# Kernel optimization log

Measured on AMD Instinct MI355X. Metric: run time of the kernel, lower is better.

## Reference

```python
import jax, jax.numpy as jnp
import numpy as np

N_HEAD = 32
HEAD_DIM = 32  # must equal N_HEAD due to the module's einsum index reuse
N_EMBD = N_HEAD * HEAD_DIM
VOCAB = 32000
B, T = 2, 64
TEMP_MIN = 0.1


def setup_inputs() -> dict:
    key = jax.random.key(0)
    ks = jax.random.split(key, 8)
    inv = 1.0 / np.sqrt(HEAD_DIM)
    return {
        "x": jax.random.normal(ks[0], (B, T, N_EMBD), dtype=jnp.float32),
        "vocab_emb": jax.random.normal(ks[1], (VOCAB, N_EMBD), dtype=jnp.float32) * 0.02,
        "W_ffn": jax.random.normal(ks[2], (HEAD_DIM, HEAD_DIM), dtype=jnp.float32) * inv,
        "b_ffn": jnp.zeros((HEAD_DIM,), dtype=jnp.float32),
        "temps": jnp.ones((N_HEAD,), dtype=jnp.float32),
        "W_ref": jax.random.normal(ks[3], (HEAD_DIM, HEAD_DIM), dtype=jnp.float32) * inv,
        "b_ref": jnp.zeros((HEAD_DIM,), dtype=jnp.float32),
        "W_gate": jax.random.normal(ks[4], (HEAD_DIM, HEAD_DIM), dtype=jnp.float32) * inv,
        "b_gate": jnp.zeros((HEAD_DIM,), dtype=jnp.float32),
    }


def reference(x, vocab_emb, W_ffn, b_ffn, temps, W_ref, b_ref, W_gate, b_gate):
    Bs, Ts, C = x.shape
    # per-head channel decomposition: (B*T, n_head, head_dim)
    xc = x.reshape(Bs * Ts, N_HEAD, HEAD_DIM)
    # channel_ffns: shared Linear over the head_dim axis (torch Linear: x @ W.T + b)
    ffn = jnp.einsum('bnh,dh->bnd', xc, W_ffn) + b_ffn
    # vocab channels: (n_head, vocab, head_dim)
    vc = vocab_emb.reshape(VOCAB, N_HEAD, HEAD_DIM).transpose(1, 0, 2)
    temps_c = jnp.clip(temps, TEMP_MIN, None)[None, :, None]

    def vocab_project(q):
        # faithful to torch: einsum('bnh,hvd->bnv') contracts q's head_dim
        # against vc's HEAD axis and sums over d as well (requires head_dim == n_head)
        logits = jnp.einsum('bnh,hvd->bnv', q, vc)
        w = jax.nn.softmax(logits / temps_c, axis=-1)  # (B*T, n_head, vocab)
        return jnp.einsum('bnv,hvd->bnh', w, vc)

    vocab_out = vocab_project(ffn)  # (B*T, n_head, head_dim)

    # refinement stage (use_vocab_refinement=True)
    refinement = jnp.tanh(jnp.einsum('bnh,dh->bnd', xc, W_ref) + b_ref)
    gate = jax.nn.sigmoid(jnp.einsum('bnh,dh->bnd', xc, W_gate) + b_gate)
    refined = vocab_out * (1.0 - gate) + refinement * gate
    vocab_out = vocab_project(refined)

    # dropout p=0 (eval) -> identity
    return vocab_out.reshape(Bs, Ts, C)
```

## Files before the change

### kernel.cpp

```cpp
#include <hip/hip_runtime.h>
#include <hip/hip_bf16.h>
#include <cstdint>

typedef unsigned int uint;
typedef unsigned short ushort_t;

typedef __attribute__((ext_vector_type(8))) short short8;
typedef __attribute__((ext_vector_type(4))) short short4_t;
typedef __attribute__((ext_vector_type(4))) float float4_t;

#define NEMBD 1024
#define VOCAB 32000
#define LOG2E 1.4426950408889634f

__device__ __forceinline__ ushort_t f2bf_rne(float f) {
    uint u = __float_as_uint(f);
    u += 0x7fffu + ((u >> 16) & 1u);
    return (ushort_t)(u >> 16);
}

__global__ void k_build_st(const float* __restrict__ ve, ushort_t* __restrict__ ST) {
    int v = blockIdx.x;
    int t = threadIdx.x;
    const float4* row = (const float4*)(ve + (size_t)v * NEMBD);
    float4 f = row[t];
    float s = f.x + f.y + f.z + f.w;
    s += __shfl_down(s, 4, 8);
    s += __shfl_down(s, 2, 8);
    s += __shfl_down(s, 1, 8);
    if ((t & 7) == 0) ST[v * 32 + (t >> 3)] = f2bf_rne(s);
}

__global__ void k_pack(const ushort_t* __restrict__ ST, ushort_t* __restrict__ SA,
                       ushort_t* __restrict__ S2) {
    int c = blockIdx.x;
    int t = threadIdx.x;
    if (t < 128) {
        int tile = t >> 6, lane = t & 63;
        int quad = lane >> 4, lo = lane & 15;
        uint4 d = *(const uint4*)(ST + ((size_t)(c * 32 + tile * 16 + lo)) * 32 + quad * 8);
        ((uint4*)SA)[c * 128 + t] = d;
    } else {
        int tt = t - 128;
        int f = tt >> 6, l = tt & 63;
        int quad = l >> 4, lo = l & 15;
        uint w[4];
        #pragma unroll
        for (int t2 = 0; t2 < 2; t2++) {
            #pragma unroll
            for (int jj = 0; jj < 2; jj++) {
                ushort_t v0 = ST[(c * 32 + t2 * 16 + quad * 4 + jj * 2 + 0) * 32 + f * 16 + lo];
                ushort_t v1 = ST[(c * 32 + t2 * 16 + quad * 4 + jj * 2 + 1) * 32 + f * 16 + lo];
                w[t2 * 2 + jj] = (uint)v0 | ((uint)v1 << 16);
            }
        }
        ((uint4*)S2)[c * 128 + tt] = make_uint4(w[0], w[1], w[2], w[3]);
    }
}

__global__ void k_q1(const float* __restrict__ x, const float* __restrict__ W,
                     const float* __restrict__ b, const float* __restrict__ temps,
                     ushort_t* __restrict__ q1) {
    int tid = blockIdx.x * 256 + threadIdx.x;
    int i = tid >> 5, d = tid & 31, n = i & 31;
    const float* xr = x + i * 32;
    float s = b[d];
    #pragma unroll
    for (int h = 0; h < 32; h++) s += xr[h] * W[d * 32 + h];
    q1[tid] = f2bf_rne(s * (LOG2E / fmaxf(temps[n], 0.1f)));
}

__launch_bounds__(256, 8)
__global__ void k_proj(const ushort_t* __restrict__ SA, const ushort_t* __restrict__ S2,
                       const ushort_t* __restrict__ q, float* __restrict__ pN,
                       float* __restrict__ pD) {
    __shared__ ushort_t buf[2][2][2048];
    int g = blockIdx.x >> 5, p = blockIdx.x & 31;
    int w = threadIdx.x >> 6, lane = threadIdx.x & 63;
    int quad = lane >> 4, lo = lane & 15;

    short8 qf = *(const short8*)(q + ((g * 64 + w * 16 + lo) * 32 + quad * 8));

    float4_t pv0 = (float4_t){0.f, 0.f, 0.f, 0.f};
    float4_t pv1 = (float4_t){0.f, 0.f, 0.f, 0.f};
    float dsum = 0.f;
    const float4_t zero4 = (float4_t){0.f, 0.f, 0.f, 0.f};

    int start = (p * 125) >> 2, end = ((p + 1) * 125) >> 2;

    {
        int c = start + (w >> 1);
        if (c < end) {
            const ushort_t* src = ((w & 1) ? S2 : SA) + (size_t)c * 1024;
            uint4 d0 = *(const uint4*)(src + lane * 8);
            uint4 d1 = *(const uint4*)(src + 512 + lane * 8);
            uint4* dst = (uint4*)(&buf[0][w >> 1][(w & 1) * 1024]);
            dst[lane] = d0;
            dst[64 + lane] = d1;
        }
    }
    __syncthreads();

    int ngrp = (end - start + 1) >> 1;
    for (int grp = 0; grp < ngrp; grp++) {
        int cur = grp & 1;
        int cn = start + (grp + 1) * 2 + (w >> 1);
        if (cn < end) {
            const ushort_t* src = ((w & 1) ? S2 : SA) + (size_t)cn * 1024;
            uint4 d0 = *(const uint4*)(src + lane * 8);
            uint4 d1 = *(const uint4*)(src + 512 + lane * 8);
            uint4* dst = (uint4*)(&buf[cur ^ 1][w >> 1][(w & 1) * 1024]);
            dst[lane] = d0;
            dst[64 + lane] = d1;
        }
        int c0 = start + grp * 2;
        int jend = (end - c0 < 2) ? (end - c0) : 2;
        for (int j = 0; j < jend; j++) {
            const ushort_t* sa = &buf[cur][j][0];
            const ushort_t* s2 = &buf[cur][j][1024];
            short8 a0 = *(const short8*)(sa + lane * 8);
            short8 a1 = *(const short8*)(sa + 512 + lane * 8);
            short8 sb0 = *(const short8*)(s2 + lane * 8);
            short8 sb1 = *(const short8*)(s2 + 512 + lane * 8);
            short4_t b00 = {sb0[0], sb0[1], sb0[2], sb0[3]};
            short4_t b01 = {sb0[4], sb0[5], sb0[6], sb0[7]};
            short4_t b10 = {sb1[0], sb1[1], sb1[2], sb1[3]};
            short4_t b11 = {sb1[4], sb1[5], sb1[6], sb1[7]};

            float4_t l0 = __builtin_amdgcn_mfma_f32_16x16x32_bf16(a0, qf, zero4, 0, 0, 0);
            float4_t l1 = __builtin_amdgcn_mfma_f32_16x16x32_bf16(a1, qf, zero4, 0, 0, 0);
            float e0 = __builtin_amdgcn_exp2f(l0[0]);
            float e1 = __builtin_amdgcn_exp2f(l0[1]);
            float e2 = __builtin_amdgcn_exp2f(l0[2]);
            float e3 = __builtin_amdgcn_exp2f(l0[3]);
            float f0 = __builtin_amdgcn_exp2f(l1[0]);
            float f1 = __builtin_amdgcn_exp2f(l1[1]);
            float f2 = __builtin_amdgcn_exp2f(l1[2]);
            float f3 = __builtin_amdgcn_exp2f(l1[3]);
            uint u0 = __builtin_amdgcn_perm(__float_as_uint(e1), __float_as_uint(e0), 0x07060302u);
            uint u1 = __builtin_amdgcn_perm(__float_as_uint(e3), __float_as_uint(e2), 0x07060302u);
            uint u2 = __builtin_amdgcn_perm(__float_as_uint(f1), __float_as_uint(f0), 0x07060302u);
            uint u3 = __builtin_amdgcn_perm(__float_as_uint(f3), __float_as_uint(f2), 0x07060302u);
            dsum += __uint_as_float(u0 << 16) + __uint_as_float(u0 & 0xffff0000u)
                  + __uint_as_float(u1 << 16) + __uint_as_float(u1 & 0xffff0000u)
                  + __uint_as_float(u2 << 16) + __uint_as_float(u2 & 0xffff0000u)
                  + __uint_as_float(u3 << 16) + __uint_as_float(u3 & 0xffff0000u);
            union { uint u[2]; short4_t s4; } c0u, c1u;
            c0u.u[0] = u0; c0u.u[1] = u1;
            c1u.u[0] = u2; c1u.u[1] = u3;
            short4_t P0 = c0u.s4, P1 = c1u.s4;
            pv0 = __builtin_amdgcn_mfma_f32_16x16x16bf16_1k(P0, b00, pv0, 0, 0, 0);
            pv0 = __builtin_amdgcn_mfma_f32_16x16x16bf16_1k(P1, b01, pv0, 0, 0, 0);
            pv1 = __builtin_amdgcn_mfma_f32_16x16x16bf16_1k(P0, b10, pv1, 0, 0, 0);
            pv1 = __builtin_amdgcn_mfma_f32_16x16x16bf16_1k(P1, b11, pv1, 0, 0, 0);
        }
        __syncthreads();
    }

    dsum += __shfl_xor(dsum, 16, 64);
    dsum += __shfl_xor(dsum, 32, 64);

    int gp = blockIdx.x;
    #pragma unroll
    for (int r = 0; r < 4; r++) {
        int ql = w * 16 + quad * 4 + r;
        pN[((size_t)gp * 64 + ql) * 32 + lo]      = pv0[r];
        pN[((size_t)gp * 64 + ql) * 32 + 16 + lo] = pv1[r];
    }
    if (quad == 0) pD[gp * 64 + w * 16 + lo] = dsum;
}

__global__ void k_refine(const float* __restrict__ pN, const float* __restrict__ pD,
                         const float* __restrict__ x,
                         const float* __restrict__ Wr, const float* __restrict__ br,
                         const float* __restrict__ Wg, const float* __restrict__ bg,
                         const float* __restrict__ temps, ushort_t* __restrict__ q2) {
    int tid = blockIdx.x * 256 + threadIdx.x;
    int i = tid >> 5, h = tid & 31, n = i & 31;
    int g = i >> 6, ql = i & 63;
    float N = 0.f, D = 0.f;
    #pragma unroll
    for (int p = 0; p < 32; p++) {
        N += pN[((size_t)(g * 32 + p) * 64 + ql) * 32 + h];
        D += pD[(g * 32 + p) * 64 + ql];
    }
    float vo = N / D;
    const float* xr = x + i * 32;
    float sr = br[h], sg = bg[h];
    #pragma unroll
    for (int h2 = 0; h2 < 32; h2++) {
        sr += xr[h2] * Wr[h * 32 + h2];
        sg += xr[h2] * Wg[h * 32 + h2];
    }
    float ref  = tanhf(sr);
    float gate = 1.f / (1.f + __expf(-sg));
    float refined = vo * (1.f - gate) + ref * gate;
    q2[tid] = f2bf_rne(refined * (LOG2E / fmaxf(temps[n], 0.1f)));
}

__global__ void k_final(const float* __restrict__ pN, const float* __restrict__ pD,
                        float* __restrict__ out) {
    int tid = blockIdx.x * 256 + threadIdx.x;
    int i = tid >> 5, h = tid & 31;
    int g = i >> 6, ql = i & 63;
    float N = 0.f, D = 0.f;
    #pragma unroll
    for (int p = 0; p < 32; p++) {
        N += pN[((size_t)(g * 32 + p) * 64 + ql) * 32 + h];
        D += pD[(g * 32 + p) * 64 + ql];
    }
    out[tid] = N / D;
}

extern "C" void kernel_launch(void* const* d_in, const int* in_sizes, int n_in,
                              void* d_out, int out_size, void* d_ws, size_t ws_size,
                              hipStream_t stream) {
    const float* x     = (const float*)d_in[0];
    const float* ve    = (const float*)d_in[1];
    const float* Wf    = (const float*)d_in[2];
    const float* bfn   = (const float*)d_in[3];
    const float* temps = (const float*)d_in[4];
    const float* Wr    = (const float*)d_in[5];
    const float* br    = (const float*)d_in[6];
    const float* Wg    = (const float*)d_in[7];
    const float* bg    = (const float*)d_in[8];
    float* out = (float*)d_out;

    char* ws = (char*)d_ws;
    ushort_t* ST = (ushort_t*)ws;
    ushort_t* SA = (ushort_t*)(ws + 2048000);
    ushort_t* S2 = (ushort_t*)(ws + 4096000);
    ushort_t* q1 = (ushort_t*)(ws + 6144000);
    ushort_t* q2 = (ushort_t*)(ws + 6144000 + 262144);
    char* base = ws + 6144000 + 2 * 262144;
    float* pNa = (float*)base;
    float* pDa = (float*)(base + 16777216);
    float* pNb = (float*)(base + 16777216 + 524288);
    float* pDb = (float*)(base + 2 * 16777216 + 524288);

    k_build_st<<<dim3(VOCAB), dim3(256), 0, stream>>>(ve, ST);
    k_pack<<<dim3(1000), dim3(256), 0, stream>>>(ST, SA, S2);
    k_q1<<<dim3(512), dim3(256), 0, stream>>>(x, Wf, bfn, temps, q1);
    k_proj<<<dim3(2048), dim3(256), 0, stream>>>(SA, S2, q1, pNa, pDa);
    k_refine<<<dim3(512), dim3(256), 0, stream>>>(pNa, pDa, x, Wr, br, Wg, bg, temps, q2);
    k_proj<<<dim3(2048), dim3(256), 0, stream>>>(SA, S2, q2, pNb, pDb);
    k_final<<<dim3(512), dim3(256), 0, stream>>>(pNb, pDb, out);
}
```

Baseline: 276.4 us.

## Drop LDS staging in k_proj, read vocab tiles directly, reorder block mapping

Removes the double-buffered shared-memory staging and per-group barriers in the projection kernel. Each wave now loads its vocab tile fragments straight from global memory with an unrolled loop. The block index mapping is swapped so that the 64 query groups sharing a vocab partition run as neighbouring blocks, which should improve L2 reuse of the vocab slice. The reduction kernels are updated to the new partial-result layout. The risk is that every wave now issues redundant global loads and loses latency hiding, since the barriers previously kept the waves in step.

New measurement: 286.7 us. +3.7%, slower.

```diff
diff --git a/kernel.cpp b/kernel.cpp
--- a/kernel.cpp
+++ b/kernel.cpp
@@ -74,8 +74,7 @@
 __global__ void k_proj(const ushort_t* __restrict__ SA, const ushort_t* __restrict__ S2,
                        const ushort_t* __restrict__ q, float* __restrict__ pN,
                        float* __restrict__ pD) {
-    __shared__ ushort_t buf[2][2][2048];
-    int g = blockIdx.x >> 5, p = blockIdx.x & 31;
+    int p = blockIdx.x >> 6, g = blockIdx.x & 63;
     int w = threadIdx.x >> 6, lane = threadIdx.x & 63;
     int quad = lane >> 4, lo = lane & 15;
 
@@ -87,74 +86,47 @@
     const float4_t zero4 = (float4_t){0.f, 0.f, 0.f, 0.f};
 
     int start = (p * 125) >> 2, end = ((p + 1) * 125) >> 2;
-
-    {
-        int c = start + (w >> 1);
-        if (c < end) {
-            const ushort_t* src = ((w & 1) ? S2 : SA) + (size_t)c * 1024;
-            uint4 d0 = *(const uint4*)(src + lane * 8);
-            uint4 d1 = *(const uint4*)(src + 512 + lane * 8);
-            uint4* dst = (uint4*)(&buf[0][w >> 1][(w & 1) * 1024]);
-            dst[lane] = d0;
-            dst[64 + lane] = d1;
-        }
-    }
-    __syncthreads();
-
-    int ngrp = (end - start + 1) >> 1;
-    for (int grp = 0; grp < ngrp; grp++) {
-        int cur = grp & 1;
-        int cn = start + (grp + 1) * 2 + (w >> 1);
-        if (cn < end) {
-            const ushort_t* src = ((w & 1) ? S2 : SA) + (size_t)cn * 1024;
-            uint4 d0 = *(const uint4*)(src + lane * 8);
-            uint4 d1 = *(const uint4*)(src + 512 + lane * 8);
-            uint4* dst = (uint4*)(&buf[cur ^ 1][w >> 1][(w & 1) * 1024]);
-            dst[lane] = d0;
-            dst[64 + lane] = d1;
-        }
-        int c0 = start + grp * 2;
-        int jend = (end - c0 < 2) ? (end - c0) : 2;
-        for (int j = 0; j < jend; j++) {
-            const ushort_t* sa = &buf[cur][j][0];
-            const ushort_t* s2 = &buf[cur][j][1024];
-            short8 a0 = *(const short8*)(sa + lane * 8);
-            short8 a1 = *(const short8*)(sa + 512 + lane * 8);
-            short8 sb0 = *(const short8*)(s2 + lane * 8);
-            short8 sb1 = *(const short8*)(s2 + 512 + lane * 8);
-            short4_t b00 = {sb0[0], sb0[1], sb0[2], sb0[3]};
-            short4_t b01 = {sb0[4], sb0[5], sb0[6], sb0[7]};
-            short4_t b10 = {sb1[0], sb1[1], sb1[2], sb1[3]};
-            short4_t b11 = {sb1[4], sb1[5], sb1[6], sb1[7]};
-
-            float4_t l0 = __builtin_amdgcn_mfma_f32_16x16x32_bf16(a0, qf, zero4, 0, 0, 0);
-            float4_t l1 = __builtin_amdgcn_mfma_f32_16x16x32_bf16(a1, qf, zero4, 0, 0, 0);
-            float e0 = __builtin_amdgcn_exp2f(l0[0]);
-            float e1 = __builtin_amdgcn_exp2f(l0[1]);
-            float e2 = __builtin_amdgcn_exp2f(l0[2]);
-            float e3 = __builtin_amdgcn_exp2f(l0[3]);
-            float f0 = __builtin_amdgcn_exp2f(l1[0]);
-            float f1 = __builtin_amdgcn_exp2f(l1[1]);
-            float f2 = __builtin_amdgcn_exp2f(l1[2]);
-            float f3 = __builtin_amdgcn_exp2f(l1[3]);
-            uint u0 = __builtin_amdgcn_perm(__float_as_uint(e1), __float_as_uint(e0), 0x07060302u);
-            uint u1 = __builtin_amdgcn_perm(__float_as_uint(e3), __float_as_uint(e2), 0x07060302u);
-            uint u2 = __builtin_amdgcn_perm(__float_as_uint(f1), __float_as_uint(f0), 0x07060302u);
-            uint u3 = __builtin_amdgcn_perm(__float_as_uint(f3), __float_as_uint(f2), 0x07060302u);
-            dsum += __uint_as_float(u0 << 16) + __uint_as_float(u0 & 0xffff0000u)
-                  + __uint_as_float(u1 << 16) + __uint_as_float(u1 & 0xffff0000u)
-                  + __uint_as_float(u2 << 16) + __uint_as_float(u2 & 0xffff0000u)
-                  + __uint_as_float(u3 << 16) + __uint_as_float(u3 & 0xffff0000u);
-            union { uint u[2]; short4_t s4; } c0u, c1u;
-            c0u.u[0] = u0; c0u.u[1] = u1;
-            c1u.u[0] = u2; c1u.u[1] = u3;
-            short4_t P0 = c0u.s4, P1 = c1u.s4;
-            pv0 = __builtin_amdgcn_mfma_f32_16x16x16bf16_1k(P0, b00, pv0, 0, 0, 0);
-            pv0 = __builtin_amdgcn_mfma_f32_16x16x16bf16_1k(P1, b01, pv0, 0, 0, 0);
-            pv1 = __builtin_amdgcn_mfma_f32_16x16x16bf16_1k(P0, b10, pv1, 0, 0, 0);
-            pv1 = __builtin_amdgcn_mfma_f32_16x16x16bf16_1k(P1, b11, pv1, 0, 0, 0);
-        }
-        __syncthreads();
+    const ushort_t* pa = SA + (size_t)start * 1024 + lane * 8;
+    const ushort_t* pb = S2 + (size_t)start * 1024 + lane * 8;
+
+    #pragma unroll 2
+    for (int c = start; c < end; c++) {
+        short8 a0  = *(const short8*)pa;
+        short8 a1  = *(const short8*)(pa + 512);
+        short8 sb0 = *(const short8*)pb;
+        short8 sb1 = *(const short8*)(pb + 512);
+        pa += 1024; pb += 1024;
+        short4_t b00 = {sb0[0], sb0[1], sb0[2], sb0[3]};
+        short4_t b01 = {sb0[4], sb0[5], sb0[6], sb0[7]};
+        short4_t b10 = {sb1[0], sb1[1], sb1[2], sb1[3]};
+        short4_t b11 = {sb1[4], sb1[5], sb1[6], sb1[7]};
+
+        float4_t l0 = __builtin_amdgcn_mfma_f32_16x16x32_bf16(a0, qf, zero4, 0, 0, 0);
+        float4_t l1 = __builtin_amdgcn_mfma_f32_16x16x32_bf16(a1, qf, zero4, 0, 0, 0);
+        float e0 = __builtin_amdgcn_exp2f(l0[0]);
+        float e1 = __builtin_amdgcn_exp2f(l0[1]);
+        float e2 = __builtin_amdgcn_exp2f(l0[2]);
+        float e3 = __builtin_amdgcn_exp2f(l0[3]);
+        float f0 = __builtin_amdgcn_exp2f(l1[0]);
+        float f1 = __builtin_amdgcn_exp2f(l1[1]);
+        float f2 = __builtin_amdgcn_exp2f(l1[2]);
+        float f3 = __builtin_amdgcn_exp2f(l1[3]);
+        uint u0 = __builtin_amdgcn_perm(__float_as_uint(e1), __float_as_uint(e0), 0x07060302u);
+        uint u1 = __builtin_amdgcn_perm(__float_as_uint(e3), __float_as_uint(e2), 0x07060302u);
+        uint u2 = __builtin_amdgcn_perm(__float_as_uint(f1), __float_as_uint(f0), 0x07060302u);
+        uint u3 = __builtin_amdgcn_perm(__float_as_uint(f3), __float_as_uint(f2), 0x07060302u);
+        dsum += __uint_as_float(u0 << 16) + __uint_as_float(u0 & 0xffff0000u)
+              + __uint_as_float(u1 << 16) + __uint_as_float(u1 & 0xffff0000u)
+              + __uint_as_float(u2 << 16) + __uint_as_float(u2 & 0xffff0000u)
+              + __uint_as_float(u3 << 16) + __uint_as_float(u3 & 0xffff0000u);
+        union { uint u[2]; short4_t s4; } c0u, c1u;
+        c0u.u[0] = u0; c0u.u[1] = u1;
+        c1u.u[0] = u2; c1u.u[1] = u3;
+        short4_t P0 = c0u.s4, P1 = c1u.s4;
+        pv0 = __builtin_amdgcn_mfma_f32_16x16x16bf16_1k(P0, b00, pv0, 0, 0, 0);
+        pv0 = __builtin_amdgcn_mfma_f32_16x16x16bf16_1k(P1, b01, pv0, 0, 0, 0);
+        pv1 = __builtin_amdgcn_mfma_f32_16x16x16bf16_1k(P0, b10, pv1, 0, 0, 0);
+        pv1 = __builtin_amdgcn_mfma_f32_16x16x16bf16_1k(P1, b11, pv1, 0, 0, 0);
     }
 
     dsum += __shfl_xor(dsum, 16, 64);
@@ -181,8 +153,8 @@
     float N = 0.f, D = 0.f;
     #pragma unroll
     for (int p = 0; p < 32; p++) {
-        N += pN[((size_t)(g * 32 + p) * 64 + ql) * 32 + h];
-        D += pD[(g * 32 + p) * 64 + ql];
+        N += pN[((size_t)(p * 64 + g) * 64 + ql) * 32 + h];
+        D += pD[(p * 64 + g) * 64 + ql];
     }
     float vo = N / D;
     const float* xr = x + i * 32;
@@ -206,8 +178,8 @@
     float N = 0.f, D = 0.f;
     #pragma unroll
     for (int p = 0; p < 32; p++) {
-        N += pN[((size_t)(g * 32 + p) * 64 + ql) * 32 + h];
-        D += pD[(g * 32 + p) * 64 + ql];
+        N += pN[((size_t)(p * 64 + g) * 64 + ql) * 32 + h];
+        D += pD[(p * 64 + g) * 64 + ql];
     }
     out[tid] = N / D;
 }
```
